# Kernel tuning notes

Hardware: AMD Instinct MI355X
Metric: run time of the kernel (lower is better)

## Reference

```python
import jax, jax.numpy as jnp
import numpy as np

NUM_HEADS = 16
HEAD_DIM = 128
POLY_ORDER = 4
LRPE_BASE = 10000.0
EPS = 1e-6


def _rope(x, offset=0):
    # x: [b, n, h, d] -- Lrpe type-1 rotary position embedding per head dim
    d = x.shape[-1]
    half = d // 2
    theta = LRPE_BASE ** (-jnp.arange(half, dtype=jnp.float32) * 2.0 / d)  # [half]
    pos = jnp.arange(x.shape[1], dtype=jnp.float32) + offset               # [n]
    ang = pos[:, None] * theta[None, :]                                    # [n, half]
    cos = jnp.cos(ang)[None, :, None, :]
    sin = jnp.sin(ang)[None, :, None, :]
    x1, x2 = x[..., :half], x[..., half:]
    return jnp.concatenate([x1 * cos - x2 * sin, x1 * sin + x2 * cos], axis=-1)


def setup_inputs() -> dict:
    key = jax.random.key(0)
    ks = jax.random.split(key, 5)
    b, n, d = 2, 2048, 2048
    std = 0.02  # init_std from module
    x = jax.random.normal(ks[0], (b, n, d), dtype=jnp.float32)
    Wq = jax.random.normal(ks[1], (d, d), dtype=jnp.float32) * std
    Wk = jax.random.normal(ks[2], (d, d), dtype=jnp.float32) * std
    Wv = jax.random.normal(ks[3], (d, d), dtype=jnp.float32) * std
    Wo = jax.random.normal(ks[4], (d, d), dtype=jnp.float32) * std
    return {"x": x, "Wq": Wq, "Wk": Wk, "Wv": Wv, "Wo": Wo}


def reference(x, Wq, Wk, Wv, Wo):
    b, n, d = x.shape
    h, hd = NUM_HEADS, HEAD_DIM
    # projections (nn.Linear: x @ W.T)
    q = (x @ Wq.T).reshape(b, n, h, hd)
    k = (x @ Wk.T).reshape(b, n, h, hd)
    v = (x @ Wv.T).reshape(b, n, h, hd)
    # LRPE (rotary, type 1), offset = 0 (no cache)
    q = _rope(q)
    k = _rope(k)
    # polynomial (non-softmax) attention: scores = (q.k)^p, causal mask,
    # row-normalized (linear-attention-style denominator)
    scores = jnp.einsum("bnhd,bmhd->bhnm", q, k) ** POLY_ORDER  # p=4 even -> >=0
    causal = jnp.tril(jnp.ones((n, n), dtype=scores.dtype))
    scores = scores * causal
    denom = jnp.maximum(scores.sum(-1, keepdims=True), EPS)      # [b,h,n,1]
    out = jnp.einsum("bhnm,bmhd->bhnd", scores, v) / denom        # [b,h,n,hd]
    out = out.transpose(0, 2, 1, 3).reshape(b, n, d)              # b n (h d)
    return out @ Wo.T
```

## Files before the change

### kernel.cpp

```cpp
#include <hip/hip_runtime.h>


typedef __bf16 bf16;
typedef __bf16 bf16x8 __attribute__((ext_vector_type(8)));
typedef __bf16 bf16x4 __attribute__((ext_vector_type(4)));
typedef float f32x4 __attribute__((ext_vector_type(4)));

#define GLD(g, l)                                                   \
  __builtin_amdgcn_global_load_lds(                                 \
      (const __attribute__((address_space(1))) void*)(g),           \
      (__attribute__((address_space(3))) void*)(l), 16, 0, 0)

#define MFMA(a, b, c) __builtin_amdgcn_mfma_f32_16x16x32_bf16(a, b, c, 0, 0, 0)

__global__ __launch_bounds__(256) void k_cvt(const float* __restrict__ in,
                                             bf16* __restrict__ out, int n4) {
  int i = blockIdx.x * 256 + threadIdx.x;
  if (i >= n4) return;
  float4 v = reinterpret_cast<const float4*>(in)[i];
  bf16x4 o = {(bf16)v.x, (bf16)v.y, (bf16)v.z, (bf16)v.w};
  reinterpret_cast<bf16x4*>(out)[i] = o;
}

__global__ __launch_bounds__(256) void k_cvt3(const float* __restrict__ a,
                                              const float* __restrict__ b,
                                              const float* __restrict__ c,
                                              bf16* __restrict__ out) {
  int i = blockIdx.x * 256 + threadIdx.x;
  const float* src = (i < 1048576) ? a : ((i < 2097152) ? b : c);
  int off = i & 1048575;
  float4 v = reinterpret_cast<const float4*>(src)[off];
  bf16x4 o = {(bf16)v.x, (bf16)v.y, (bf16)v.z, (bf16)v.w};
  reinterpret_cast<bf16x4*>(out)[i] = o;
}

__global__ __launch_bounds__(256) void k_rope_tab(float* __restrict__ ct,
                                                  float* __restrict__ st) {
  int i = blockIdx.x * 256 + threadIdx.x;
  if (i >= 2048 * 64) return;
  int pos = i >> 6, f = i & 63;
  float theta = exp2f(-(float)f * 0.20762050593046014f);
  float ang = (float)pos * theta;
  ct[i] = cosf(ang);
  st[i] = sinf(ang);
}

__global__ __launch_bounds__(256, 2) void k_gemm_qkv(
    const bf16* __restrict__ Am, const bf16* __restrict__ Bm,
    bf16* __restrict__ Qp, bf16* __restrict__ Kp, bf16* __restrict__ Vt,
    const float* __restrict__ ct, const float* __restrict__ st) {
  __shared__ __align__(16) char LDS[73728];
  const int tid = threadIdx.x, w = tid >> 6, l = tid & 63;
  const int lr = l & 15, g = l >> 4;
  const int wr = w >> 1, wc = w & 1;
  const int tm = blockIdx.y * 256, tn = blockIdx.x * 128;

  const int rl = tid >> 2;
  const int scol = (((tid & 3) ^ (rl & 3) ^ ((rl >> 2) & 3)) << 3);
  const int xo = ((g ^ (lr & 3) ^ ((lr >> 2) & 3)) << 4);

#define STAGEQ(buf, kt)                                                      \
  {                                                                          \
    _Pragma("unroll") for (int i = 0; i < 4; ++i)                            \
        GLD(Am + (size_t)(tm + i * 64 + rl) * 2048 + (kt) + scol,            \
            LDS + (buf) * 24576 + i * 4096 + tid * 16);                      \
    _Pragma("unroll") for (int i = 0; i < 2; ++i)                            \
        GLD(Bm + (size_t)(tn + i * 64 + rl) * 2048 + (kt) + scol,            \
            LDS + (buf) * 24576 + 16384 + i * 4096 + tid * 16);              \
  }

  f32x4 acc[8][4] = {};

  STAGEQ(0, 0);
  STAGEQ(1, 32);
  int cur = 0, st3 = 2;
  for (int t = 0; t < 63; ++t) {
    asm volatile("s_waitcnt vmcnt(6)" ::: "memory");
    __builtin_amdgcn_s_barrier();
    asm volatile("" ::: "memory");
    if (t < 62) STAGEQ(st3, (t + 2) * 32);
    const char* pa = LDS + cur * 24576;
    const char* pb = pa + 16384;
    bf16x8 a[8], b[4];
#pragma unroll
    for (int fm = 0; fm < 8; ++fm)
      a[fm] = *reinterpret_cast<const bf16x8*>(pa + (wr * 128 + fm * 16 + lr) * 64 + xo);
#pragma unroll
    for (int nf = 0; nf < 4; ++nf)
      b[nf] = *reinterpret_cast<const bf16x8*>(pb + (wc * 64 + nf * 16 + lr) * 64 + xo);
    __builtin_amdgcn_s_setprio(1);
#pragma unroll
    for (int fm = 0; fm < 8; ++fm)
#pragma unroll
      for (int nf = 0; nf < 4; ++nf)
        acc[fm][nf] = MFMA(a[fm], b[nf], acc[fm][nf]);
    __builtin_amdgcn_s_setprio(0);
    cur = (cur == 2) ? 0 : cur + 1;
    st3 = (st3 == 2) ? 0 : st3 + 1;
  }
  {
    asm volatile("s_waitcnt vmcnt(0)" ::: "memory");
    __builtin_amdgcn_s_barrier();
    asm volatile("" ::: "memory");
    const char* pa = LDS + cur * 24576;
    const char* pb = pa + 16384;
    bf16x8 a[8], b[4];
#pragma unroll
    for (int fm = 0; fm < 8; ++fm)
      a[fm] = *reinterpret_cast<const bf16x8*>(pa + (wr * 128 + fm * 16 + lr) * 64 + xo);
#pragma unroll
    for (int nf = 0; nf < 4; ++nf)
      b[nf] = *reinterpret_cast<const bf16x8*>(pb + (wc * 64 + nf * 16 + lr) * 64 + xo);
#pragma unroll
    for (int fm = 0; fm < 8; ++fm)
#pragma unroll
      for (int nf = 0; nf < 4; ++nf)
        acc[fm][nf] = MFMA(a[fm], b[nf], acc[fm][nf]);
  }

  if (tn < 4096) {
    __syncthreads();
    bf16* E = (bf16*)LDS;
#pragma unroll
    for (int fm = 0; fm < 8; ++fm)
#pragma unroll
      for (int nf = 0; nf < 4; ++nf)
#pragma unroll
        for (int rr = 0; rr < 4; ++rr)
          E[(wr * 128 + fm * 16 + g * 4 + rr) * 136 + wc * 64 + nf * 16 + lr] =
              (bf16)acc[fm][nf][rr];
    __syncthreads();
    const int hh = (tn & 2047) >> 7;
    bf16* dst = (tn < 2048) ? Qp : Kp;
#pragma unroll
    for (int i = 0; i < 16; ++i) {
      int task = i * 256 + tid;
      int row = task >> 4, dg = (task & 15) << 2;
      int token = tm + row, nn = token & 2047, bb = token >> 11;
      f32x4 c4 = *reinterpret_cast<const f32x4*>(ct + nn * 64 + dg);
      f32x4 s4 = *reinterpret_cast<const f32x4*>(st + nn * 64 + dg);
      bf16x4 x1 = *reinterpret_cast<const bf16x4*>(E + row * 136 + dg);
      bf16x4 x2 = *reinterpret_cast<const bf16x4*>(E + row * 136 + 64 + dg);
      bf16x4 o1, o2;
#pragma unroll
      for (int j = 0; j < 4; ++j) {
        float a1 = (float)x1[j], a2 = (float)x2[j];
        o1[j] = (bf16)(a1 * c4[j] - a2 * s4[j]);
        o2[j] = (bf16)(a1 * s4[j] + a2 * c4[j]);
      }
      size_t rb = (((size_t)bb * 16 + hh) * 2048 + nn) * 128;
      *reinterpret_cast<bf16x4*>(dst + rb + dg) = o1;
      *reinterpret_cast<bf16x4*>(dst + rb + 64 + dg) = o2;
    }
  } else {
#pragma unroll
    for (int fm = 0; fm < 8; ++fm)
#pragma unroll
      for (int nf = 0; nf < 4; ++nf) {
        int row0 = tm + wr * 128 + fm * 16 + g * 4;
        int col = (tn - 4096) + wc * 64 + nf * 16 + lr;
        int bb = row0 >> 11, nn = row0 & 2047;
        int hh = col >> 7, dd = col & 127;
        bf16x4 o = {(bf16)acc[fm][nf][0], (bf16)acc[fm][nf][1],
                    (bf16)acc[fm][nf][2], (bf16)acc[fm][nf][3]};
        *reinterpret_cast<bf16x4*>(
            Vt + (((size_t)bb * 16 + hh) * 128 + dd) * 2048 + nn) = o;
      }
  }
}

__global__ __launch_bounds__(256, 3) void k_gemm_out(const bf16* __restrict__ Am,
                                                     const bf16* __restrict__ Bm,
                                                     float* __restrict__ C) {
  __shared__ __align__(16) char LDS[49152];
  const int tid = threadIdx.x, w = tid >> 6, l = tid & 63;
  const int lr = l & 15, g = l >> 4;
  const int wr = w >> 1, wc = w & 1;
  const int tm = blockIdx.y * 128, tn = blockIdx.x * 128;

  const int rl = tid >> 2;
  const int scol = (((tid & 3) ^ (rl & 3) ^ ((rl >> 2) & 3)) << 3);
  const int xo = ((g ^ (lr & 3) ^ ((lr >> 2) & 3)) << 4);

#define STAGEO(buf, kt)                                                      \
  {                                                                          \
    _Pragma("unroll") for (int i = 0; i < 2; ++i)                            \
        GLD(Am + (size_t)(tm + i * 64 + rl) * 2048 + (kt) + scol,            \
            LDS + (buf) * 16384 + i * 4096 + tid * 16);                      \
    _Pragma("unroll") for (int i = 0; i < 2; ++i)                            \
        GLD(Bm + (size_t)(tn + i * 64 + rl) * 2048 + (kt) + scol,            \
            LDS + (buf) * 16384 + 8192 + i * 4096 + tid * 16);               \
  }

  f32x4 acc[4][4] = {};

  STAGEO(0, 0);
  STAGEO(1, 32);
  int cur = 0, st3 = 2;
  for (int t = 0; t < 63; ++t) {
    asm volatile("s_waitcnt vmcnt(4)" ::: "memory");
    __builtin_amdgcn_s_barrier();
    asm volatile("" ::: "memory");
    if (t < 62) STAGEO(st3, (t + 2) * 32);
    const char* pa = LDS + cur * 16384;
    const char* pb = pa + 8192;
    bf16x8 a[4], b[4];
#pragma unroll
    for (int fm = 0; fm < 4; ++fm)
      a[fm] = *reinterpret_cast<const bf16x8*>(pa + (wr * 64 + fm * 16 + lr) * 64 + xo);
#pragma unroll
    for (int nf = 0; nf < 4; ++nf)
      b[nf] = *reinterpret_cast<const bf16x8*>(pb + (wc * 64 + nf * 16 + lr) * 64 + xo);
    __builtin_amdgcn_s_setprio(1);
#pragma unroll
    for (int fm = 0; fm < 4; ++fm)
#pragma unroll
      for (int nf = 0; nf < 4; ++nf)
        acc[fm][nf] = MFMA(a[fm], b[nf], acc[fm][nf]);
    __builtin_amdgcn_s_setprio(0);
    cur = (cur == 2) ? 0 : cur + 1;
    st3 = (st3 == 2) ? 0 : st3 + 1;
  }
  {
    asm volatile("s_waitcnt vmcnt(0)" ::: "memory");
    __builtin_amdgcn_s_barrier();
    asm volatile("" ::: "memory");
    const char* pa = LDS + cur * 16384;
    const char* pb = pa + 8192;
    bf16x8 a[4], b[4];
#pragma unroll
    for (int fm = 0; fm < 4; ++fm)
      a[fm] = *reinterpret_cast<const bf16x8*>(pa + (wr * 64 + fm * 16 + lr) * 64 + xo);
#pragma unroll
    for (int nf = 0; nf < 4; ++nf)
      b[nf] = *reinterpret_cast<const bf16x8*>(pb + (wc * 64 + nf * 16 + lr) * 64 + xo);
#pragma unroll
    for (int fm = 0; fm < 4; ++fm)
#pragma unroll
      for (int nf = 0; nf < 4; ++nf)
        acc[fm][nf] = MFMA(a[fm], b[nf], acc[fm][nf]);
  }

#pragma unroll
  for (int fm = 0; fm < 4; ++fm)
#pragma unroll
    for (int nf = 0; nf < 4; ++nf)
#pragma unroll
      for (int rr = 0; rr < 4; ++rr) {
        int row = tm + wr * 64 + fm * 16 + g * 4 + rr;
        int col = tn + wc * 64 + nf * 16 + lr;
        C[(size_t)row * 2048 + col] = acc[fm][nf][rr];
      }
}

__global__ __launch_bounds__(256) void k_attn(const bf16* __restrict__ Q,
                                              const bf16* __restrict__ K,
                                              const bf16* __restrict__ Vt,
                                              bf16* __restrict__ O) {
  __shared__ __align__(16) bf16 Ks[128 * 128];
  __shared__ __align__(16) bf16 Vs[128 * 128];
  __shared__ __align__(16) bf16 Ps[64 * 128];
  const int tid = threadIdx.x, w = tid >> 6, l = tid & 63;
  const int lr = l & 15, g = l >> 4;
  const int flat = blockIdx.x;
  const int pair = flat >> 5, bh = flat & 31;
  const size_t base = (size_t)bh * 2048 * 128;
  const int b_ = bh >> 4, h_ = bh & 15;

  for (int seg = 0; seg < 2; ++seg) {
    const int qt = seg ? (31 - pair) : pair;
    const int qbase = qt * 64;
    bf16x8 qf[4];
#pragma unroll
    for (int kc = 0; kc < 4; ++kc)
      qf[kc] = *reinterpret_cast<const bf16x8*>(
          Q + base + (size_t)(qbase + w * 16 + lr) * 128 + kc * 32 + g * 8);

    f32x4 on[8] = {};
    float dn[4] = {};
    const int nt = (qbase >> 7) + 1;

    for (int t = 0; t < nt; ++t) {
      const bf16* kg = K + base + (size_t)t * 128 * 128;
      const bf16* vg = Vt + base + t * 128;
#pragma unroll
      for (int r = 0; r < 8; ++r) {
        int e = r * 2048 + w * 512 + l * 8;
        int row = e >> 7, c = (e >> 3) & 15;
        int sc = ((c ^ (row & 7)) << 3);
        GLD(kg + (row << 7) + sc, Ks + r * 2048 + w * 512);
        GLD(vg + (size_t)row * 2048 + sc, Vs + r * 2048 + w * 512);
      }
      __syncthreads();

      f32x4 s[8] = {};
      __builtin_amdgcn_s_setprio(1);
#pragma unroll
      for (int kc = 0; kc < 4; ++kc)
#pragma unroll
        for (int ni = 0; ni < 8; ++ni) {
          bf16x8 kb = *reinterpret_cast<const bf16x8*>(
              Ks + ((ni * 16 + lr) << 7) + (((kc * 4 + g) ^ (lr & 7)) << 3));
          s[ni] = MFMA(qf[kc], kb, s[ni]);
        }
      __builtin_amdgcn_s_setprio(0);

      float part[4] = {};
#pragma unroll
      for (int ni = 0; ni < 8; ++ni)
#pragma unroll
        for (int r = 0; r < 4; ++r) {
          int lrow = g * 4 + r;
          int qrow = qbase + w * 16 + lrow;
          int col = t * 128 + ni * 16 + lr;
          float v = s[ni][r];
          v = (col <= qrow) ? v : 0.f;
          float v2 = v * v, v4 = v2 * v2;
          part[r] += v4;
          int chunk = ni * 2 + (lr >> 3);
          Ps[((w * 16 + lrow) << 7) + ((chunk ^ (lrow & 7)) << 3) + (lr & 7)] =
              (bf16)v4;
        }
#pragma unroll
      for (int m = 1; m < 16; m <<= 1)
#pragma unroll
        for (int r = 0; r < 4; ++r) part[r] += __shfl_xor(part[r], m, 64);
#pragma unroll
      for (int r = 0; r < 4; ++r) dn[r] += part[r];

      __builtin_amdgcn_s_setprio(1);
#pragma unroll
      for (int kc = 0; kc < 4; ++kc) {
        bf16x8 pa = *reinterpret_cast<const bf16x8*>(
            Ps + ((w * 16 + lr) << 7) + (((kc * 4 + g) ^ (lr & 7)) << 3));
#pragma unroll
        for (int ni = 0; ni < 8; ++ni) {
          bf16x8 vb = *reinterpret_cast<const bf16x8*>(
              Vs + ((ni * 16 + lr) << 7) + (((kc * 4 + g) ^ (lr & 7)) << 3));
          on[ni] = MFMA(pa, vb, on[ni]);
        }
      }
      __builtin_amdgcn_s_setprio(0);
      __syncthreads();
    }

#pragma unroll
    for (int r = 0; r < 4; ++r) {
      float inv = 1.0f / fmaxf(dn[r], 1e-6f);
      int row = qbase + w * 16 + g * 4 + r;
#pragma unroll
      for (int ni = 0; ni < 8; ++ni)
        O[((size_t)b_ * 2048 + row) * 2048 + h_ * 128 + ni * 16 + lr] =
            (bf16)(on[ni][r] * inv);
    }
  }
}

extern "C" void kernel_launch(void* const* d_in, const int* in_sizes, int n_in,
                              void* d_out, int out_size, void* d_ws, size_t ws_size,
                              hipStream_t stream) {
  const float* x  = (const float*)d_in[0];
  const float* Wq = (const float*)d_in[1];
  const float* Wk = (const float*)d_in[2];
  const float* Wv = (const float*)d_in[3];
  const float* Wo = (const float*)d_in[4];
  float* out = (float*)d_out;

  char* p = (char*)d_ws;
  bf16* xb   = (bf16*)p; p += (size_t)8388608 * 2;
  bf16* wqkv = (bf16*)p; p += (size_t)12582912 * 2;
  bf16* wob  = (bf16*)p; p += (size_t)4194304 * 2;
  bf16* Qp   = (bf16*)p; p += (size_t)8388608 * 2;
  bf16* Kp   = (bf16*)p; p += (size_t)8388608 * 2;
  bf16* Vt   = (bf16*)p; p += (size_t)8388608 * 2;
  bf16* Ob   = (bf16*)p; p += (size_t)8388608 * 2;
  float* ct  = (float*)p; p += (size_t)131072 * 4;
  float* st  = (float*)p; p += (size_t)131072 * 4;

  k_cvt<<<8192, 256, 0, stream>>>(x, xb, 2097152);
  k_cvt3<<<12288, 256, 0, stream>>>(Wq, Wk, Wv, wqkv);
  k_cvt<<<4096, 256, 0, stream>>>(Wo, wob, 1048576);
  k_rope_tab<<<512, 256, 0, stream>>>(ct, st);

  k_gemm_qkv<<<dim3(48, 16), 256, 0, stream>>>(xb, wqkv, Qp, Kp, Vt, ct, st);

  k_attn<<<512, 256, 0, stream>>>(Qp, Kp, Vt, Ob);

  k_gemm_out<<<dim3(16, 32), 256, 0, stream>>>(Ob, wob, out);
}
```

Before: 270.3 us.

## Enlarge QKV GEMM tile to 256x256 with 8 waves and split-phase double buffering

Rewrites the QKV projection GEMM to use 512-thread blocks computing 256x256 output tiles with a 64-wide K step, double-buffered LDS (128 KB), and staging interleaved between half-tile MFMA phases. A 1D grid with a swizzled block-to-tile mapping is meant to improve L2 reuse, and the larger tile raises arithmetic intensity per LDS byte. The RoPE epilogue now runs in two passes over row halves to fit the wider tile. The large LDS footprint limits occupancy to one block per CU, and the extra barriers could expose load latency.

```diff
diff --git a/kernel.cpp b/kernel.cpp
--- a/kernel.cpp
+++ b/kernel.cpp
@@ -45,120 +45,169 @@
   st[i] = sinf(ang);
 }
 
-__global__ __launch_bounds__(256, 2) void k_gemm_qkv(
+__global__ __launch_bounds__(512, 2) void k_gemm_qkv(
     const bf16* __restrict__ Am, const bf16* __restrict__ Bm,
     bf16* __restrict__ Qp, bf16* __restrict__ Kp, bf16* __restrict__ Vt,
     const float* __restrict__ ct, const float* __restrict__ st) {
-  __shared__ __align__(16) char LDS[73728];
-  const int tid = threadIdx.x, w = tid >> 6, l = tid & 63;
+  __shared__ __align__(16) char LDS[131072];
+  const int tid = threadIdx.x, l = tid & 63, w = tid >> 6;
   const int lr = l & 15, g = l >> 4;
-  const int wr = w >> 1, wc = w & 1;
-  const int tm = blockIdx.y * 256, tn = blockIdx.x * 128;
-
-  const int rl = tid >> 2;
-  const int scol = (((tid & 3) ^ (rl & 3) ^ ((rl >> 2) & 3)) << 3);
-  const int xo = ((g ^ (lr & 3) ^ ((lr >> 2) & 3)) << 4);
-
-#define STAGEQ(buf, kt)                                                      \
-  {                                                                          \
-    _Pragma("unroll") for (int i = 0; i < 4; ++i)                            \
-        GLD(Am + (size_t)(tm + i * 64 + rl) * 2048 + (kt) + scol,            \
-            LDS + (buf) * 24576 + i * 4096 + tid * 16);                      \
-    _Pragma("unroll") for (int i = 0; i < 2; ++i)                            \
-        GLD(Bm + (size_t)(tn + i * 64 + rl) * 2048 + (kt) + scol,            \
-            LDS + (buf) * 24576 + 16384 + i * 4096 + tid * 16);              \
+  const int wm = w >> 2, wn = w & 3;
+  const int bid = blockIdx.x;
+  const int swz = (bid & 7) * 48 + (bid >> 3);
+  const int tn = (swz % 24) * 256;
+  const int tm = (swz / 24) * 256;
+
+  const int clv = (tid & 7) ^ ((tid >> 3) & 7);
+  const int srow0 = 2 * (tid >> 3) + (clv >> 2);
+  const int skcol = (clv & 3) * 8;
+  const bf16* As0 = Am + (size_t)(tm + srow0) * 2048 + skcol;
+  const bf16* As1 = Am + (size_t)(tm + 128 + srow0) * 2048 + skcol;
+  const bf16* Bs0 = Bm + (size_t)(tn + srow0) * 2048 + skcol;
+  const bf16* Bs1 = Bm + (size_t)(tn + 128 + srow0) * 2048 + skcol;
+
+  const int cp = (((lr & 1) << 2) | g) ^ ((lr >> 1) & 7);
+  const int aoff = wm * 8192 + (lr >> 1) * 128 + cp * 16;
+  const int boff = wn * 4096 + (lr >> 1) * 128 + cp * 16;
+
+#define STAGE(slotoff, p0, p1, kk)                       \
+  {                                                      \
+    GLD((p0) + (kk), LDS + (slotoff) + tid * 16);        \
+    GLD((p1) + (kk), LDS + (slotoff) + 8192 + tid * 16); \
   }
 
   f32x4 acc[8][4] = {};
 
-  STAGEQ(0, 0);
-  STAGEQ(1, 32);
-  int cur = 0, st3 = 2;
-  for (int t = 0; t < 63; ++t) {
-    asm volatile("s_waitcnt vmcnt(6)" ::: "memory");
-    __builtin_amdgcn_s_barrier();
-    asm volatile("" ::: "memory");
-    if (t < 62) STAGEQ(st3, (t + 2) * 32);
-    const char* pa = LDS + cur * 24576;
-    const char* pb = pa + 16384;
-    bf16x8 a[8], b[4];
+  STAGE(0, As0, As1, 0);
+  STAGE(32768, Bs0, Bs1, 0);
+  STAGE(16384, As0, As1, 32);
+  STAGE(49152, Bs0, Bs1, 32);
+  asm volatile("s_waitcnt vmcnt(4)" ::: "memory");
+  __builtin_amdgcn_s_barrier();
+  asm volatile("" ::: "memory");
+
+  for (int t = 0; t < 32; ++t) {
+    const int c = t & 1, o = c * 65536, on = (c ^ 1) * 65536;
+    const int kn = (t + 1) * 64;
+    const bool lastT = (t == 31);
+    const char* pa0 = LDS + o;
+    const char* pa1 = LDS + o + 16384;
+    const char* pb0 = LDS + o + 32768;
+    const char* pb1 = LDS + o + 49152;
+    bf16x8 a[8], b0, b1;
+
 #pragma unroll
     for (int fm = 0; fm < 8; ++fm)
-      a[fm] = *reinterpret_cast<const bf16x8*>(pa + (wr * 128 + fm * 16 + lr) * 64 + xo);
-#pragma unroll
-    for (int nf = 0; nf < 4; ++nf)
-      b[nf] = *reinterpret_cast<const bf16x8*>(pb + (wc * 64 + nf * 16 + lr) * 64 + xo);
+      a[fm] = *reinterpret_cast<const bf16x8*>(pa0 + aoff + fm * 1024);
+    b0 = *reinterpret_cast<const bf16x8*>(pb0 + boff);
+    b1 = *reinterpret_cast<const bf16x8*>(pb0 + boff + 1024);
+    if (!lastT) STAGE(on, As0, As1, kn);
     __builtin_amdgcn_s_setprio(1);
 #pragma unroll
+    for (int fm = 0; fm < 8; ++fm) {
+      acc[fm][0] = MFMA(a[fm], b0, acc[fm][0]);
+      acc[fm][1] = MFMA(a[fm], b1, acc[fm][1]);
+    }
+    __builtin_amdgcn_s_setprio(0);
+    __builtin_amdgcn_s_barrier();
+    asm volatile("" ::: "memory");
+
+    b0 = *reinterpret_cast<const bf16x8*>(pb0 + boff + 2048);
+    b1 = *reinterpret_cast<const bf16x8*>(pb0 + boff + 3072);
+    if (!lastT) STAGE(on + 32768, Bs0, Bs1, kn);
+    __builtin_amdgcn_s_setprio(1);
+#pragma unroll
+    for (int fm = 0; fm < 8; ++fm) {
+      acc[fm][2] = MFMA(a[fm], b0, acc[fm][2]);
+      acc[fm][3] = MFMA(a[fm], b1, acc[fm][3]);
+    }
+    __builtin_amdgcn_s_setprio(0);
+    if (lastT)
+      asm volatile("s_waitcnt vmcnt(0)" ::: "memory");
+    else
+      asm volatile("s_waitcnt vmcnt(4)" ::: "memory");
+    __builtin_amdgcn_s_barrier();
+    asm volatile("" ::: "memory");
+
+#pragma unroll
     for (int fm = 0; fm < 8; ++fm)
-#pragma unroll
-      for (int nf = 0; nf < 4; ++nf)
-        acc[fm][nf] = MFMA(a[fm], b[nf], acc[fm][nf]);
+      a[fm] = *reinterpret_cast<const bf16x8*>(pa1 + aoff + fm * 1024);
+    b0 = *reinterpret_cast<const bf16x8*>(pb1 + boff);
+    b1 = *reinterpret_cast<const bf16x8*>(pb1 + boff + 1024);
+    if (!lastT) STAGE(on + 16384, As0, As1, kn + 32);
+    __builtin_amdgcn_s_setprio(1);
+#pragma unroll
+    for (int fm = 0; fm < 8; ++fm) {
+      acc[fm][0] = MFMA(a[fm], b0, acc[fm][0]);
+      acc[fm][1] = MFMA(a[fm], b1, acc[fm][1]);
+    }
     __builtin_amdgcn_s_setprio(0);
-    cur = (cur == 2) ? 0 : cur + 1;
-    st3 = (st3 == 2) ? 0 : st3 + 1;
-  }
-  {
-    asm volatile("s_waitcnt vmcnt(0)" ::: "memory");
-    __builtin_amdgcn_s_barrier();
-    asm volatile("" ::: "memory");
-    const char* pa = LDS + cur * 24576;
-    const char* pb = pa + 16384;
-    bf16x8 a[8], b[4];
+    __builtin_amdgcn_s_barrier();
+    asm volatile("" ::: "memory");
+
+    b0 = *reinterpret_cast<const bf16x8*>(pb1 + boff + 2048);
+    b1 = *reinterpret_cast<const bf16x8*>(pb1 + boff + 3072);
+    if (!lastT) STAGE(on + 49152, Bs0, Bs1, kn + 32);
+    __builtin_amdgcn_s_setprio(1);
+#pragma unroll
+    for (int fm = 0; fm < 8; ++fm) {
+      acc[fm][2] = MFMA(a[fm], b0, acc[fm][2]);
+      acc[fm][3] = MFMA(a[fm], b1, acc[fm][3]);
+    }
+    __builtin_amdgcn_s_setprio(0);
+    if (!lastT) asm volatile("s_waitcnt vmcnt(4)" ::: "memory");
+    __builtin_amdgcn_s_barrier();
+    asm volatile("" ::: "memory");
+  }
+
+  if (tn < 4096) {
+    bf16* dst = (tn < 2048) ? Qp : Kp;
+    const int nb = tn & 2047;
+    bf16* E = (bf16*)LDS;
+    for (int pass = 0; pass < 2; ++pass) {
+      __syncthreads();
+      if (wm == pass) {
+#pragma unroll
+        for (int fm = 0; fm < 8; ++fm)
+#pragma unroll
+          for (int nf = 0; nf < 4; ++nf)
+#pragma unroll
+            for (int rr = 0; rr < 4; ++rr)
+              E[(fm * 16 + g * 4 + rr) * 264 + wn * 64 + nf * 16 + lr] =
+                  (bf16)acc[fm][nf][rr];
+      }
+      __syncthreads();
+#pragma unroll
+      for (int it = 0; it < 8; ++it) {
+        int task = it * 512 + tid;
+        int row = task >> 5, rem = task & 31;
+        int hd = rem >> 4, dg = (rem & 15) << 2;
+        int token = tm + pass * 128 + row;
+        int nn = token & 2047, bb = token >> 11;
+        f32x4 c4 = *reinterpret_cast<const f32x4*>(ct + nn * 64 + dg);
+        f32x4 s4 = *reinterpret_cast<const f32x4*>(st + nn * 64 + dg);
+        bf16x4 x1 = *reinterpret_cast<const bf16x4*>(E + row * 264 + hd * 128 + dg);
+        bf16x4 x2 = *reinterpret_cast<const bf16x4*>(E + row * 264 + hd * 128 + 64 + dg);
+        bf16x4 o1, o2;
+#pragma unroll
+        for (int j = 0; j < 4; ++j) {
+          float a1 = (float)x1[j], a2 = (float)x2[j];
+          o1[j] = (bf16)(a1 * c4[j] - a2 * s4[j]);
+          o2[j] = (bf16)(a1 * s4[j] + a2 * c4[j]);
+        }
+        int h_ = (nb >> 7) + hd;
+        size_t rb = (((size_t)bb * 16 + h_) * 2048 + nn) * 128;
+        *reinterpret_cast<bf16x4*>(dst + rb + dg) = o1;
+        *reinterpret_cast<bf16x4*>(dst + rb + 64 + dg) = o2;
+      }
+    }
+  } else {
 #pragma unroll
     for (int fm = 0; fm < 8; ++fm)
-      a[fm] = *reinterpret_cast<const bf16x8*>(pa + (wr * 128 + fm * 16 + lr) * 64 + xo);
-#pragma unroll
-    for (int nf = 0; nf < 4; ++nf)
-      b[nf] = *reinterpret_cast<const bf16x8*>(pb + (wc * 64 + nf * 16 + lr) * 64 + xo);
-#pragma unroll
-    for (int fm = 0; fm < 8; ++fm)
-#pragma unroll
-      for (int nf = 0; nf < 4; ++nf)
-        acc[fm][nf] = MFMA(a[fm], b[nf], acc[fm][nf]);
-  }
-
-  if (tn < 4096) {
-    __syncthreads();
-    bf16* E = (bf16*)LDS;
-#pragma unroll
-    for (int fm = 0; fm < 8; ++fm)
-#pragma unroll
-      for (int nf = 0; nf < 4; ++nf)
-#pragma unroll
-        for (int rr = 0; rr < 4; ++rr)
-          E[(wr * 128 + fm * 16 + g * 4 + rr) * 136 + wc * 64 + nf * 16 + lr] =
-              (bf16)acc[fm][nf][rr];
-    __syncthreads();
-    const int hh = (tn & 2047) >> 7;
-    bf16* dst = (tn < 2048) ? Qp : Kp;
-#pragma unroll
-    for (int i = 0; i < 16; ++i) {
-      int task = i * 256 + tid;
-      int row = task >> 4, dg = (task & 15) << 2;
-      int token = tm + row, nn = token & 2047, bb = token >> 11;
-      f32x4 c4 = *reinterpret_cast<const f32x4*>(ct + nn * 64 + dg);
-      f32x4 s4 = *reinterpret_cast<const f32x4*>(st + nn * 64 + dg);
-      bf16x4 x1 = *reinterpret_cast<const bf16x4*>(E + row * 136 + dg);
-      bf16x4 x2 = *reinterpret_cast<const bf16x4*>(E + row * 136 + 64 + dg);
-      bf16x4 o1, o2;
-#pragma unroll
-      for (int j = 0; j < 4; ++j) {
-        float a1 = (float)x1[j], a2 = (float)x2[j];
-        o1[j] = (bf16)(a1 * c4[j] - a2 * s4[j]);
-        o2[j] = (bf16)(a1 * s4[j] + a2 * c4[j]);
-      }
-      size_t rb = (((size_t)bb * 16 + hh) * 2048 + nn) * 128;
-      *reinterpret_cast<bf16x4*>(dst + rb + dg) = o1;
-      *reinterpret_cast<bf16x4*>(dst + rb + 64 + dg) = o2;
-    }
-  } else {
-#pragma unroll
-    for (int fm = 0; fm < 8; ++fm)
 #pragma unroll
       for (int nf = 0; nf < 4; ++nf) {
-        int row0 = tm + wr * 128 + fm * 16 + g * 4;
-        int col = (tn - 4096) + wc * 64 + nf * 16 + lr;
+        int row0 = tm + wm * 128 + fm * 16 + g * 4;
+        int col = (tn - 4096) + wn * 64 + nf * 16 + lr;
         int bb = row0 >> 11, nn = row0 & 2047;
         int hh = col >> 7, dd = col & 127;
         bf16x4 o = {(bf16)acc[fm][nf][0], (bf16)acc[fm][nf][1],
@@ -382,7 +431,7 @@
   k_cvt<<<4096, 256, 0, stream>>>(Wo, wob, 1048576);
   k_rope_tab<<<512, 256, 0, stream>>>(ct, st);
 
-  k_gemm_qkv<<<dim3(48, 16), 256, 0, stream>>>(xb, wqkv, Qp, Kp, Vt, ct, st);
+  k_gemm_qkv<<<384, 512, 0, stream>>>(xb, wqkv, Qp, Kp, Vt, ct, st);
 
   k_attn<<<512, 256, 0, stream>>>(Qp, Kp, Vt, Ob);
 
```

New measurement: 277.0 us. 2.5% more time.

## Restructure QKV GEMM to 512 threads with BK=64 and interleaved staging

Applied to the files above, without the earlier changes.

The QKV projection GEMM now runs 8 waves per block (2x4 wave grid) with a K-step of 64 and a triple-buffered 144KB LDS ring. Global-to-LDS loads for the next tile are split into two halves and issued between the two MFMA sub-phases, with barriers around each. Block indices are swizzled so consecutive blocks share B columns, which should help L2 reuse. The goal is better latency hiding and MFMA utilisation, at the cost of much more LDS per block, so fewer blocks fit per CU and there are more barriers per iteration.

```diff
diff --git a/kernel.cpp b/kernel.cpp
--- a/kernel.cpp
+++ b/kernel.cpp
@@ -45,106 +45,121 @@
   st[i] = sinf(ang);
 }
 
-__global__ __launch_bounds__(256, 2) void k_gemm_qkv(
+__global__ __launch_bounds__(512, 2) void k_gemm_qkv(
     const bf16* __restrict__ Am, const bf16* __restrict__ Bm,
     bf16* __restrict__ Qp, bf16* __restrict__ Kp, bf16* __restrict__ Vt,
     const float* __restrict__ ct, const float* __restrict__ st) {
-  __shared__ __align__(16) char LDS[73728];
-  const int tid = threadIdx.x, w = tid >> 6, l = tid & 63;
+  __shared__ __align__(16) char LDS[147456];
+  const int tid = threadIdx.x, l = tid & 63, w = tid >> 6;
   const int lr = l & 15, g = l >> 4;
-  const int wr = w >> 1, wc = w & 1;
-  const int tm = blockIdx.y * 256, tn = blockIdx.x * 128;
-
-  const int rl = tid >> 2;
-  const int scol = (((tid & 3) ^ (rl & 3) ^ ((rl >> 2) & 3)) << 3);
-  const int xo = ((g ^ (lr & 3) ^ ((lr >> 2) & 3)) << 4);
-
-#define STAGEQ(buf, kt)                                                      \
-  {                                                                          \
-    _Pragma("unroll") for (int i = 0; i < 4; ++i)                            \
-        GLD(Am + (size_t)(tm + i * 64 + rl) * 2048 + (kt) + scol,            \
-            LDS + (buf) * 24576 + i * 4096 + tid * 16);                      \
-    _Pragma("unroll") for (int i = 0; i < 2; ++i)                            \
-        GLD(Bm + (size_t)(tn + i * 64 + rl) * 2048 + (kt) + scol,            \
-            LDS + (buf) * 24576 + 16384 + i * 4096 + tid * 16);              \
-  }
-
-  f32x4 acc[8][4] = {};
-
-  STAGEQ(0, 0);
-  STAGEQ(1, 32);
-  int cur = 0, st3 = 2;
-  for (int t = 0; t < 63; ++t) {
+  const int wm = w >> 2, wn = w & 3;
+  const int swz = (blockIdx.x & 7) * 96 + (blockIdx.x >> 3);
+  const int tm = (swz & 15) * 256;
+  const int tn = (swz >> 4) * 128;
+
+  const int srow = tid >> 3;
+  const int scol = ((tid & 7) ^ (srow & 7)) << 3;
+  const bf16* Au0 = Am + (size_t)(tm + srow) * 2048 + scol;
+  const bf16* Au1 = Am + (size_t)(tm + 64 + srow) * 2048 + scol;
+  const bf16* Au2 = Am + (size_t)(tm + 128 + srow) * 2048 + scol;
+  const bf16* Au3 = Am + (size_t)(tm + 192 + srow) * 2048 + scol;
+  const bf16* Bu0 = Bm + (size_t)(tn + srow) * 2048 + scol;
+  const bf16* Bu1 = Bm + (size_t)(tn + 64 + srow) * 2048 + scol;
+
+  const int x0 = ((0 + g) ^ (lr & 7)) << 4;
+  const int x1 = ((4 + g) ^ (lr & 7)) << 4;
+  const int abase = wm * 16384 + lr * 128;
+  const int bbase = 32768 + wn * 4096 + lr * 128;
+
+#define SU(dst, src, kc) GLD((src) + (kc), LDS + (dst) + tid * 16)
+#define STAGE_TILE(bb, kc)                                        \
+  {                                                               \
+    SU((bb) + 0, Au0, kc); SU((bb) + 8192, Au1, kc);              \
+    SU((bb) + 16384, Au2, kc); SU((bb) + 24576, Au3, kc);         \
+    SU((bb) + 32768, Bu0, kc); SU((bb) + 40960, Bu1, kc);         \
+  }
+
+  f32x4 acc[8][2] = {};
+
+  STAGE_TILE(0, 0);
+  STAGE_TILE(49152, 64);
+  asm volatile("s_waitcnt vmcnt(6)" ::: "memory");
+  __builtin_amdgcn_s_barrier();
+
+  int cur = 0;
+  for (int k = 0; k < 32; ++k) {
+    const int nx = ((k + 2) % 3) * 49152;
+    const int kc = (k + 2 < 32 ? k + 2 : 31) * 64;
+    const char* base = LDS + cur;
+    bf16x8 a[8], b0, b1;
+
+#pragma unroll
+    for (int fm = 0; fm < 8; ++fm)
+      a[fm] = *reinterpret_cast<const bf16x8*>(base + abase + fm * 2048 + x0);
+    b0 = *reinterpret_cast<const bf16x8*>(base + bbase + x0);
+    b1 = *reinterpret_cast<const bf16x8*>(base + bbase + 2048 + x0);
+    SU(nx + 0, Au0, kc);
+    SU(nx + 8192, Au1, kc);
+    SU(nx + 16384, Au2, kc);
+    __builtin_amdgcn_s_barrier();
+    __builtin_amdgcn_s_setprio(1);
+#pragma unroll
+    for (int fm = 0; fm < 8; ++fm) {
+      acc[fm][0] = MFMA(a[fm], b0, acc[fm][0]);
+      acc[fm][1] = MFMA(a[fm], b1, acc[fm][1]);
+    }
+    __builtin_amdgcn_s_setprio(0);
+    __builtin_amdgcn_s_barrier();
+
+#pragma unroll
+    for (int fm = 0; fm < 8; ++fm)
+      a[fm] = *reinterpret_cast<const bf16x8*>(base + abase + fm * 2048 + x1);
+    b0 = *reinterpret_cast<const bf16x8*>(base + bbase + x1);
+    b1 = *reinterpret_cast<const bf16x8*>(base + bbase + 2048 + x1);
+    SU(nx + 24576, Au3, kc);
+    SU(nx + 32768, Bu0, kc);
+    SU(nx + 40960, Bu1, kc);
+    __builtin_amdgcn_s_barrier();
+    __builtin_amdgcn_s_setprio(1);
+#pragma unroll
+    for (int fm = 0; fm < 8; ++fm) {
+      acc[fm][0] = MFMA(a[fm], b0, acc[fm][0]);
+      acc[fm][1] = MFMA(a[fm], b1, acc[fm][1]);
+    }
+    __builtin_amdgcn_s_setprio(0);
     asm volatile("s_waitcnt vmcnt(6)" ::: "memory");
     __builtin_amdgcn_s_barrier();
-    asm volatile("" ::: "memory");
-    if (t < 62) STAGEQ(st3, (t + 2) * 32);
-    const char* pa = LDS + cur * 24576;
-    const char* pb = pa + 16384;
-    bf16x8 a[8], b[4];
+    cur = (cur == 98304) ? 0 : cur + 49152;
+  }
+  asm volatile("s_waitcnt vmcnt(0)" ::: "memory");
+  __builtin_amdgcn_s_barrier();
+
+  if (tn < 4096) {
+    bf16* E = (bf16*)LDS;
 #pragma unroll
     for (int fm = 0; fm < 8; ++fm)
-      a[fm] = *reinterpret_cast<const bf16x8*>(pa + (wr * 128 + fm * 16 + lr) * 64 + xo);
-#pragma unroll
-    for (int nf = 0; nf < 4; ++nf)
-      b[nf] = *reinterpret_cast<const bf16x8*>(pb + (wc * 64 + nf * 16 + lr) * 64 + xo);
-    __builtin_amdgcn_s_setprio(1);
-#pragma unroll
-    for (int fm = 0; fm < 8; ++fm)
-#pragma unroll
-      for (int nf = 0; nf < 4; ++nf)
-        acc[fm][nf] = MFMA(a[fm], b[nf], acc[fm][nf]);
-    __builtin_amdgcn_s_setprio(0);
-    cur = (cur == 2) ? 0 : cur + 1;
-    st3 = (st3 == 2) ? 0 : st3 + 1;
-  }
-  {
-    asm volatile("s_waitcnt vmcnt(0)" ::: "memory");
-    __builtin_amdgcn_s_barrier();
-    asm volatile("" ::: "memory");
-    const char* pa = LDS + cur * 24576;
-    const char* pb = pa + 16384;
-    bf16x8 a[8], b[4];
-#pragma unroll
-    for (int fm = 0; fm < 8; ++fm)
-      a[fm] = *reinterpret_cast<const bf16x8*>(pa + (wr * 128 + fm * 16 + lr) * 64 + xo);
-#pragma unroll
-    for (int nf = 0; nf < 4; ++nf)
-      b[nf] = *reinterpret_cast<const bf16x8*>(pb + (wc * 64 + nf * 16 + lr) * 64 + xo);
-#pragma unroll
-    for (int fm = 0; fm < 8; ++fm)
-#pragma unroll
-      for (int nf = 0; nf < 4; ++nf)
-        acc[fm][nf] = MFMA(a[fm], b[nf], acc[fm][nf]);
-  }
-
-  if (tn < 4096) {
-    __syncthreads();
-    bf16* E = (bf16*)LDS;
-#pragma unroll
-    for (int fm = 0; fm < 8; ++fm)
-#pragma unroll
-      for (int nf = 0; nf < 4; ++nf)
+#pragma unroll
+      for (int nf = 0; nf < 2; ++nf)
 #pragma unroll
         for (int rr = 0; rr < 4; ++rr)
-          E[(wr * 128 + fm * 16 + g * 4 + rr) * 136 + wc * 64 + nf * 16 + lr] =
+          E[(wm * 128 + fm * 16 + g * 4 + rr) * 136 + wn * 32 + nf * 16 + lr] =
               (bf16)acc[fm][nf][rr];
     __syncthreads();
     const int hh = (tn & 2047) >> 7;
     bf16* dst = (tn < 2048) ? Qp : Kp;
 #pragma unroll
-    for (int i = 0; i < 16; ++i) {
-      int task = i * 256 + tid;
+    for (int it = 0; it < 8; ++it) {
+      int task = it * 512 + tid;
       int row = task >> 4, dg = (task & 15) << 2;
       int token = tm + row, nn = token & 2047, bb = token >> 11;
       f32x4 c4 = *reinterpret_cast<const f32x4*>(ct + nn * 64 + dg);
       f32x4 s4 = *reinterpret_cast<const f32x4*>(st + nn * 64 + dg);
-      bf16x4 x1 = *reinterpret_cast<const bf16x4*>(E + row * 136 + dg);
-      bf16x4 x2 = *reinterpret_cast<const bf16x4*>(E + row * 136 + 64 + dg);
+      bf16x4 x1v = *reinterpret_cast<const bf16x4*>(E + row * 136 + dg);
+      bf16x4 x2v = *reinterpret_cast<const bf16x4*>(E + row * 136 + 64 + dg);
       bf16x4 o1, o2;
 #pragma unroll
       for (int j = 0; j < 4; ++j) {
-        float a1 = (float)x1[j], a2 = (float)x2[j];
+        float a1 = (float)x1v[j], a2 = (float)x2v[j];
         o1[j] = (bf16)(a1 * c4[j] - a2 * s4[j]);
         o2[j] = (bf16)(a1 * s4[j] + a2 * c4[j]);
       }
@@ -156,9 +171,9 @@
 #pragma unroll
     for (int fm = 0; fm < 8; ++fm)
 #pragma unroll
-      for (int nf = 0; nf < 4; ++nf) {
-        int row0 = tm + wr * 128 + fm * 16 + g * 4;
-        int col = (tn - 4096) + wc * 64 + nf * 16 + lr;
+      for (int nf = 0; nf < 2; ++nf) {
+        int row0 = tm + wm * 128 + fm * 16 + g * 4;
+        int col = (tn - 4096) + wn * 32 + nf * 16 + lr;
         int bb = row0 >> 11, nn = row0 & 2047;
         int hh = col >> 7, dd = col & 127;
         bf16x4 o = {(bf16)acc[fm][nf][0], (bf16)acc[fm][nf][1],
@@ -382,7 +397,7 @@
   k_cvt<<<4096, 256, 0, stream>>>(Wo, wob, 1048576);
   k_rope_tab<<<512, 256, 0, stream>>>(ct, st);
 
-  k_gemm_qkv<<<dim3(48, 16), 256, 0, stream>>>(xb, wqkv, Qp, Kp, Vt, ct, st);
+  k_gemm_qkv<<<768, 512, 0, stream>>>(xb, wqkv, Qp, Kp, Vt, ct, st);
 
   k_attn<<<512, 256, 0, stream>>>(Qp, Kp, Vt, Ob);
 
```

Result: slower. 276.3 us (+2.2%).
